# Kernel optimization log

Hardware: AMD Instinct MI355X
Metric: run time of the kernel (lower is better)

Reference implementation:

```python
import jax, jax.numpy as jnp
import numpy as np

D_MODEL = 256
N_LEVELS = 4
N_HEADS = 8
N_POINTS = 4
D_HEAD = D_MODEL // N_HEADS  # 32
BATCH = 8
SHAPES = np.array([[64, 64], [32, 32], [16, 16], [8, 8]], dtype=np.int32)
LEN_IN = int((SHAPES[:, 0] * SHAPES[:, 1]).sum())  # 5440
LEN_Q = LEN_IN
STARTS = np.concatenate([[0], np.cumsum(SHAPES[:, 0] * SHAPES[:, 1])[:-1]]).astype(np.int32)


def _offset_bias():
    # faithful _reset_parameters grid init for sampling_offsets bias
    thetas = np.arange(N_HEADS, dtype=np.float64) * (2.0 * np.pi / N_HEADS)
    grid = np.stack([np.cos(thetas), np.sin(thetas)], -1)
    grid = grid / np.abs(grid).max(-1, keepdims=True)
    grid = np.tile(grid[:, None, None, :], (1, N_LEVELS, N_POINTS, 1))
    grid = grid * (np.arange(N_POINTS) + 1)[None, None, :, None]
    return jnp.asarray(grid.reshape(-1), dtype=jnp.float32)


def setup_inputs() -> dict:
    key = jax.random.key(0)
    ks = jax.random.split(key, 8)
    s = 1.0 / np.sqrt(D_MODEL)
    return {
        "query": jax.random.normal(ks[0], (BATCH, LEN_Q, D_MODEL), jnp.float32),
        "reference_points": jax.random.uniform(ks[1], (BATCH, LEN_Q, N_LEVELS, 2), jnp.float32),
        "input_flatten": jax.random.normal(ks[2], (BATCH, LEN_IN, D_MODEL), jnp.float32),
        "input_spatial_shapes": jnp.asarray(SHAPES),
        "input_level_start_index": jnp.asarray(STARTS),
        "W_val": jax.random.normal(ks[3], (D_MODEL, D_MODEL), jnp.float32) * s,
        "b_val": jnp.zeros((D_MODEL,), jnp.float32),
        "W_off": jax.random.normal(ks[4], (D_MODEL, N_HEADS * N_LEVELS * N_POINTS * 2), jnp.float32) * 0.01,
        "b_off": _offset_bias(),
        "W_attn": jax.random.normal(ks[5], (D_MODEL, N_HEADS * N_LEVELS * N_POINTS), jnp.float32) * s,
        "b_attn": jnp.zeros((N_HEADS * N_LEVELS * N_POINTS,), jnp.float32),
        "W_out": jax.random.normal(ks[6], (D_MODEL, D_MODEL), jnp.float32) * s,
        "b_out": jnp.zeros((D_MODEL,), jnp.float32),
    }


def _ms_deform_attn_core(value, shapes_np, starts_np, sampling_locations, attention_weights):
    # value: (N, Lin, Hn, d); sampling_locations: (N, Lq, Hn, L, P, 2) in [0,1]
    # attention_weights: (N, Lq, Hn, L, P)
    n, lq = sampling_locations.shape[:2]
    value_t = jnp.transpose(value, (0, 2, 1, 3))  # (N, Hn, Lin, d)
    out = jnp.zeros((n, N_HEADS, lq, value.shape[-1]), value.dtype)
    for lvl in range(N_LEVELS):
        H, W = int(shapes_np[lvl, 0]), int(shapes_np[lvl, 1])
        st = int(starts_np[lvl])
        v = value_t[:, :, st:st + H * W]  # (N, Hn, H*W, d)
        loc = jnp.transpose(sampling_locations[:, :, :, lvl], (0, 2, 1, 3, 4))  # (N, Hn, Lq, P, 2)
        x = loc[..., 0] * W - 0.5
        y = loc[..., 1] * H - 0.5
        x0 = jnp.floor(x).astype(jnp.int32)
        y0 = jnp.floor(y).astype(jnp.int32)
        lx = x - x0
        ly = y - y0
        x1, y1 = x0 + 1, y0 + 1

        def gather(yc, xc):
            valid = (yc >= 0) & (yc < H) & (xc >= 0) & (xc < W)
            idx = jnp.clip(yc, 0, H - 1) * W + jnp.clip(xc, 0, W - 1)
            idx = idx.reshape(n, N_HEADS, -1)  # (N, Hn, Lq*P)
            g = jnp.take_along_axis(v, idx[..., None], axis=2)  # (N, Hn, Lq*P, d)
            return g * valid.reshape(n, N_HEADS, -1, 1)

        w00 = ((1 - lx) * (1 - ly)).reshape(n, N_HEADS, -1, 1)
        w01 = (lx * (1 - ly)).reshape(n, N_HEADS, -1, 1)
        w10 = ((1 - lx) * ly).reshape(n, N_HEADS, -1, 1)
        w11 = (lx * ly).reshape(n, N_HEADS, -1, 1)
        samp = (gather(y0, x0) * w00 + gather(y0, x1) * w01 +
                gather(y1, x0) * w10 + gather(y1, x1) * w11)
        samp = samp.reshape(n, N_HEADS, lq, N_POINTS, -1)
        aw = jnp.transpose(attention_weights[:, :, :, lvl], (0, 2, 1, 3))  # (N, Hn, Lq, P)
        out = out + (samp * aw[..., None]).sum(axis=3)
    return jnp.transpose(out, (0, 2, 1, 3)).reshape(n, lq, -1)


def reference(query, reference_points, input_flatten, input_spatial_shapes,
              input_level_start_index, W_val, b_val, W_off, b_off,
              W_attn, b_attn, W_out, b_out):
    shapes_np = np.asarray(input_spatial_shapes)
    starts_np = np.asarray(input_level_start_index)
    n, lq, _ = query.shape
    lin = input_flatten.shape[1]

    value = (input_flatten @ W_val + b_val).reshape(n, lin, N_HEADS, D_HEAD)
    off = (query @ W_off + b_off).reshape(n, lq, N_HEADS, N_LEVELS, N_POINTS, 2)
    attn = jax.nn.softmax((query @ W_attn + b_attn).reshape(n, lq, N_HEADS, N_LEVELS * N_POINTS), axis=-1)
    attn = attn.reshape(n, lq, N_HEADS, N_LEVELS, N_POINTS)

    # normalizer: (L, 2) as [W, H]
    normalizer = jnp.stack([input_spatial_shapes[:, 1], input_spatial_shapes[:, 0]], -1).astype(query.dtype)
    loc = reference_points[:, :, None, :, None, :] + off / normalizer[None, None, None, :, None, :]

    out = _ms_deform_attn_core(value, shapes_np, starts_np, loc, attn)
    return out @ W_out + b_out
```

## Files before the change

### kernel.cpp

```cpp
#include <hip/hip_runtime.h>

typedef unsigned short ushort;
typedef unsigned int uint;
typedef __bf16 bf16x8 __attribute__((ext_vector_type(8)));
typedef float floatx4 __attribute__((ext_vector_type(4)));
typedef ushort ushort8 __attribute__((ext_vector_type(8)));

constexpr int LQ = 5440;
constexpr int ROWS = 43520;

__device__ __forceinline__ ushort f2b(float f) {
  union { float f; uint i; } v; v.f = f;
  uint r = v.i + 0x7FFFu + ((v.i >> 16) & 1u);
  return (ushort)(r >> 16);
}
__device__ __forceinline__ float blo(uint u) {
  union { uint i; float f; } v; v.i = u << 16; return v.f;
}
__device__ __forceinline__ float bhi(uint u) {
  union { uint i; float f; } v; v.i = u & 0xFFFF0000u; return v.f;
}

__global__ __launch_bounds__(256) void wcast_kernel(
    const float* __restrict__ Wv, const float* __restrict__ Wo,
    const float* __restrict__ Wa, const float* __restrict__ Wu,
    ushort* __restrict__ Wt) {
  int k = threadIdx.x;
  int n = blockIdx.x;
  int m = blockIdx.y;
  const float* src = (m == 0) ? Wv : (m == 1) ? Wo : (m == 2) ? Wa : Wu;
  int N = (m == 2) ? 128 : 256;
  if (n >= N) return;
  size_t off = (size_t)m * 65536 - ((m == 3) ? 32768 : 0);
  Wt[off + (size_t)n * 256 + k] = f2b(src[(size_t)k * N + n]);
}

template<bool F2B>
__device__ __forceinline__ void mfma_tile128(
    const void* __restrict__ Av, const ushort* __restrict__ Bt,
    int row_base, int n0, ushort* At, ushort* Bs, floatx4 (&acc)[4][4]) {
  const int t = threadIdx.x;
  const int lane = t & 63, wv = t >> 6;
  const int quad = lane >> 4, l15 = lane & 15;
  const int mt0 = (wv >> 1) * 4, nt0 = (wv & 1) * 4;
#pragma unroll
  for (int i = 0; i < 4; ++i)
#pragma unroll
    for (int j = 0; j < 4; ++j) acc[i][j] = floatx4{0.f, 0.f, 0.f, 0.f};

  for (int k0 = 0; k0 < 256; k0 += 32) {
#pragma unroll
    for (int i = 0; i < 2; ++i) {
      int item = t + 256 * i;
      int r = item >> 2, q = item & 3;
      int slot = ((r >> 4) * 64 + q * 16 + (r & 15)) * 8;
      if (F2B) {
        const float* ap = (const float*)Av + (size_t)(row_base + r) * 256 + k0 + q * 8;
        float4 a0 = *(const float4*)ap, a1 = *(const float4*)(ap + 4);
        ushort8 u;
        u[0] = f2b(a0.x); u[1] = f2b(a0.y); u[2] = f2b(a0.z); u[3] = f2b(a0.w);
        u[4] = f2b(a1.x); u[5] = f2b(a1.y); u[6] = f2b(a1.z); u[7] = f2b(a1.w);
        *(ushort8*)&At[slot] = u;
      } else {
        const ushort* ap = (const ushort*)Av + (size_t)(row_base + r) * 256 + k0 + q * 8;
        *(ushort8*)&At[slot] = *(const ushort8*)ap;
      }
    }
#pragma unroll
    for (int i = 0; i < 2; ++i) {
      int item = t + 256 * i;
      int nr = item >> 2, q = item & 3;
      int slot = ((nr >> 4) * 64 + q * 16 + (nr & 15)) * 8;
      *(ushort8*)&Bs[slot] = *(const ushort8*)(Bt + (size_t)(n0 + nr) * 256 + k0 + q * 8);
    }
    __syncthreads();
    bf16x8 af[4], bfv[4];
#pragma unroll
    for (int ti = 0; ti < 4; ++ti)
      af[ti] = *(const bf16x8*)&At[((mt0 + ti) * 64 + lane) * 8];
#pragma unroll
    for (int tj = 0; tj < 4; ++tj)
      bfv[tj] = *(const bf16x8*)&Bs[((nt0 + tj) * 64 + lane) * 8];
#pragma unroll
    for (int ti = 0; ti < 4; ++ti)
#pragma unroll
      for (int tj = 0; tj < 4; ++tj)
        acc[ti][tj] = __builtin_amdgcn_mfma_f32_16x16x32_bf16(af[ti], bfv[tj], acc[ti][tj], 0, 0, 0);
    __syncthreads();
  }
}

__global__ __launch_bounds__(256) void gemm_val_kernel(
    const float* __restrict__ X, const ushort* __restrict__ WtV,
    const float* __restrict__ bval, ushort* __restrict__ value16) {
  __shared__ ushort At[8192];
  __shared__ ushort Bs[8192];
  floatx4 acc[4][4];
  int row_base = blockIdx.x * 128, n0 = blockIdx.y * 128;
  mfma_tile128<true>(X, WtV, row_base, n0, At, Bs, acc);
  const int t = threadIdx.x, lane = t & 63, wv = t >> 6;
  const int quad = lane >> 4, l15 = lane & 15;
  const int mt0 = (wv >> 1) * 4, nt0 = (wv & 1) * 4;
#pragma unroll
  for (int tj = 0; tj < 4; ++tj) {
    int gcol = n0 + (nt0 + tj) * 16 + l15;
    float b = bval[gcol];
#pragma unroll
    for (int ti = 0; ti < 4; ++ti)
#pragma unroll
      for (int reg = 0; reg < 4; ++reg) {
        int grow = row_base + (mt0 + ti) * 16 + quad * 4 + reg;
        value16[(size_t)grow * 256 + gcol] = f2b(acc[ti][tj][reg] + b);
      }
  }
}

__global__ __launch_bounds__(256) void gemm_oa_kernel(
    const float* __restrict__ Q, const ushort* __restrict__ WtOA,
    const float* __restrict__ boff, const float* __restrict__ battn,
    const float* __restrict__ refp, uint4* __restrict__ tblq) {
  __shared__ ushort At[2048];
  __shared__ ushort Bs[12288];
  const int t = threadIdx.x;
  const int lane = t & 63, wv = t >> 6;
  const int quad = lane >> 4, l15 = lane & 15;
  int row_base = blockIdx.x * 64;
  floatx4 accO[4][4];
  floatx4 accA[2][4];
#pragma unroll
  for (int p = 0; p < 4; ++p)
#pragma unroll
    for (int ti = 0; ti < 4; ++ti) accO[p][ti] = floatx4{0.f, 0.f, 0.f, 0.f};
#pragma unroll
  for (int q = 0; q < 2; ++q)
#pragma unroll
    for (int ti = 0; ti < 4; ++ti) accA[q][ti] = floatx4{0.f, 0.f, 0.f, 0.f};

  for (int k0 = 0; k0 < 256; k0 += 32) {
    {
      int r = t >> 2, q = t & 3;
      const float* ap = Q + (size_t)(row_base + r) * 256 + k0 + q * 8;
      float4 a0 = *(const float4*)ap, a1 = *(const float4*)(ap + 4);
      ushort8 u;
      u[0] = f2b(a0.x); u[1] = f2b(a0.y); u[2] = f2b(a0.z); u[3] = f2b(a0.w);
      u[4] = f2b(a1.x); u[5] = f2b(a1.y); u[6] = f2b(a1.z); u[7] = f2b(a1.w);
      *(ushort8*)&At[((r >> 4) * 64 + q * 16 + (r & 15)) * 8] = u;
    }
#pragma unroll
    for (int i = 0; i < 6; ++i) {
      int item = t + 256 * i;
      int nr = item >> 2, q = item & 3;
      *(ushort8*)&Bs[((nr >> 4) * 64 + q * 16 + (nr & 15)) * 8] =
          *(const ushort8*)(WtOA + (size_t)nr * 256 + k0 + q * 8);
    }
    __syncthreads();
    bf16x8 af[4];
#pragma unroll
    for (int ti = 0; ti < 4; ++ti)
      af[ti] = *(const bf16x8*)&At[(ti * 64 + lane) * 8];
#pragma unroll
    for (int p = 0; p < 4; ++p) {
      bf16x8 bf = *(const bf16x8*)&Bs[(((4 * wv + p)) * 64 + lane) * 8];
#pragma unroll
      for (int ti = 0; ti < 4; ++ti)
        accO[p][ti] = __builtin_amdgcn_mfma_f32_16x16x32_bf16(af[ti], bf, accO[p][ti], 0, 0, 0);
    }
#pragma unroll
    for (int q = 0; q < 2; ++q) {
      bf16x8 bf = *(const bf16x8*)&Bs[((16 + 2 * wv + q) * 64 + lane) * 8];
#pragma unroll
      for (int ti = 0; ti < 4; ++ti)
        accA[q][ti] = __builtin_amdgcn_mfma_f32_16x16x32_bf16(af[ti], bf, accA[q][ti], 0, 0, 0);
    }
    __syncthreads();
  }

  float boO[4], boA[2];
#pragma unroll
  for (int p = 0; p < 4; ++p) boO[p] = boff[(4 * wv + p) * 16 + l15];
#pragma unroll
  for (int q = 0; q < 2; ++q) boA[q] = battn[(2 * wv + q) * 16 + l15];
  const int lp = l15, l = lp >> 2;
  const int wd = 64 >> l;
  const int st = (l == 0) ? 0 : (l == 1) ? 4096 : (l == 2) ? 5120 : 5376;
  const float lw = (float)wd;
  const int src = (quad << 4) | (2 * (lp & 7));

#pragma unroll
  for (int ti = 0; ti < 4; ++ti)
#pragma unroll
    for (int reg = 0; reg < 4; ++reg) {
      int grow = row_base + ti * 16 + quad * 4 + reg;
      float rx = refp[(size_t)grow * 8 + l * 2];
      float ry = refp[(size_t)grow * 8 + l * 2 + 1];
#pragma unroll
      for (int hh = 0; hh < 2; ++hh) {
        int h = 2 * wv + hh;
        float xa = accA[hh][ti][reg] + boA[hh];
        float m = xa;
        m = fmaxf(m, __shfl_xor(m, 1, 64));
        m = fmaxf(m, __shfl_xor(m, 2, 64));
        m = fmaxf(m, __shfl_xor(m, 4, 64));
        m = fmaxf(m, __shfl_xor(m, 8, 64));
        float e = __expf(xa - m);
        float ssum = e;
        ssum += __shfl_xor(ssum, 1, 64);
        ssum += __shfl_xor(ssum, 2, 64);
        ssum += __shfl_xor(ssum, 4, 64);
        ssum += __shfl_xor(ssum, 8, 64);
        float aw = e / ssum;
        float v0 = accO[2 * hh][ti][reg] + boO[2 * hh];
        float v1 = accO[2 * hh + 1][ti][reg] + boO[2 * hh + 1];
        float x_lo = __shfl(v0, src, 64),     x_hi = __shfl(v1, src, 64);
        float y_lo = __shfl(v0, src | 1, 64), y_hi = __shfl(v1, src | 1, 64);
        float xo = (lp < 8) ? x_lo : x_hi;
        float yo = (lp < 8) ? y_lo : y_hi;
        float X = rx * lw + xo - 0.5f;
        float Y = ry * lw + yo - 0.5f;
        float fx = floorf(X), fy = floorf(Y);
        float lx = X - fx, ly = Y - fy;
        int x0 = (int)fx, y0 = (int)fy, x1 = x0 + 1, y1 = y0 + 1;
        int cx0 = min(max(x0, 0), wd - 1), cx1 = min(max(x1, 0), wd - 1);
        int cy0 = min(max(y0, 0), wd - 1), cy1 = min(max(y1, 0), wd - 1);
        float vx0 = (x0 >= 0 && x0 < wd) ? 1.f : 0.f;
        float vx1 = (x1 >= 0 && x1 < wd) ? 1.f : 0.f;
        float vy0 = (y0 >= 0 && y0 < wd) ? 1.f : 0.f;
        float vy1 = (y1 >= 0 && y1 < wd) ? 1.f : 0.f;
        float g00 = (1.f - lx) * (1.f - ly) * vx0 * vy0 * aw;
        float g01 = lx * (1.f - ly) * vx1 * vy0 * aw;
        float g10 = (1.f - lx) * ly * vx0 * vy1 * aw;
        float g11 = lx * ly * vx1 * vy1 * aw;
        uint i00 = st + cy0 * wd + cx0, i01 = st + cy0 * wd + cx1;
        uint i10 = st + cy1 * wd + cx0, i11 = st + cy1 * wd + cx1;
        uint4 ov;
        ov.x = i00 | (i01 << 16);
        ov.y = i10 | (i11 << 16);
        ov.z = (uint)f2b(g00) | ((uint)f2b(g01) << 16);
        ov.w = (uint)f2b(g10) | ((uint)f2b(g11) << 16);
        tblq[((size_t)grow * 8 + h) * 16 + lp] = ov;
      }
    }
}

__global__ __launch_bounds__(512) void core_kernel(
    const ushort* __restrict__ value16, const uint4* __restrict__ tblq,
    uint* __restrict__ coreo32) {
  const int bx = blockIdx.x;
  const int b = bx & 7;
  const int brow = b * LQ + (bx >> 3);
  const int t = threadIdx.x;
  const int h = t >> 6, lane = t & 63;
  const int s = lane >> 3, g = lane & 7;
  const size_t sbase = ((size_t)brow * 8 + h) * 16;
  uint4 sl0 = tblq[sbase + s];
  uint4 sl1 = tblq[sbase + s + 8];
  const uint2* vb = (const uint2*)value16 + (size_t)b * (LQ * 64) + h * 8 + g;
  float a0 = 0.f, a1 = 0.f, a2 = 0.f, a3 = 0.f;
#pragma unroll
  for (int lpi = 0; lpi < 2; ++lpi) {
    uint4 sl = lpi ? sl1 : sl0;
    uint2 v00 = vb[(size_t)(sl.x & 0xFFFFu) * 64];
    uint2 v01 = vb[(size_t)(sl.x >> 16) * 64];
    uint2 v10 = vb[(size_t)(sl.y & 0xFFFFu) * 64];
    uint2 v11 = vb[(size_t)(sl.y >> 16) * 64];
    float w00 = blo(sl.z), w01 = bhi(sl.z), w10 = blo(sl.w), w11 = bhi(sl.w);
    a0 = fmaf(w00, blo(v00.x), a0); a1 = fmaf(w00, bhi(v00.x), a1);
    a2 = fmaf(w00, blo(v00.y), a2); a3 = fmaf(w00, bhi(v00.y), a3);
    a0 = fmaf(w01, blo(v01.x), a0); a1 = fmaf(w01, bhi(v01.x), a1);
    a2 = fmaf(w01, blo(v01.y), a2); a3 = fmaf(w01, bhi(v01.y), a3);
    a0 = fmaf(w10, blo(v10.x), a0); a1 = fmaf(w10, bhi(v10.x), a1);
    a2 = fmaf(w10, blo(v10.y), a2); a3 = fmaf(w10, bhi(v10.y), a3);
    a0 = fmaf(w11, blo(v11.x), a0); a1 = fmaf(w11, bhi(v11.x), a1);
    a2 = fmaf(w11, blo(v11.y), a2); a3 = fmaf(w11, bhi(v11.y), a3);
  }
#pragma unroll
  for (int m = 8; m <= 32; m <<= 1) {
    a0 += __shfl_xor(a0, m, 64);
    a1 += __shfl_xor(a1, m, 64);
    a2 += __shfl_xor(a2, m, 64);
    a3 += __shfl_xor(a3, m, 64);
  }
  if (s == 0) {
    uint2 o;
    o.x = (uint)f2b(a0) | ((uint)f2b(a1) << 16);
    o.y = (uint)f2b(a2) | ((uint)f2b(a3) << 16);
    *(uint2*)(coreo32 + (size_t)brow * 128 + h * 16 + g * 2) = o;
  }
}

__global__ __launch_bounds__(256) void gemm_out_kernel(
    const ushort* __restrict__ C, const ushort* __restrict__ WtU,
    const float* __restrict__ bout, float* __restrict__ out) {
  __shared__ ushort At[8192];
  __shared__ ushort Bs[8192];
  floatx4 acc[4][4];
  int row_base = blockIdx.x * 128, n0 = blockIdx.y * 128;
  mfma_tile128<false>(C, WtU, row_base, n0, At, Bs, acc);
  const int t = threadIdx.x, lane = t & 63, wv = t >> 6;
  const int quad = lane >> 4, l15 = lane & 15;
  const int mt0 = (wv >> 1) * 4, nt0 = (wv & 1) * 4;
#pragma unroll
  for (int tj = 0; tj < 4; ++tj) {
    int gcol = n0 + (nt0 + tj) * 16 + l15;
    float b = bout[gcol];
#pragma unroll
    for (int ti = 0; ti < 4; ++ti)
#pragma unroll
      for (int reg = 0; reg < 4; ++reg) {
        int grow = row_base + (mt0 + ti) * 16 + quad * 4 + reg;
        out[(size_t)grow * 256 + gcol] = acc[ti][tj][reg] + b;
      }
  }
}

extern "C" void kernel_launch(void* const* d_in, const int* in_sizes, int n_in,
                              void* d_out, int out_size, void* d_ws, size_t ws_size,
                              hipStream_t stream) {
  const float* query  = (const float*)d_in[0];
  const float* refp   = (const float*)d_in[1];
  const float* inpf   = (const float*)d_in[2];
  const float* W_val  = (const float*)d_in[5];
  const float* b_val  = (const float*)d_in[6];
  const float* W_off  = (const float*)d_in[7];
  const float* b_off  = (const float*)d_in[8];
  const float* W_attn = (const float*)d_in[9];
  const float* b_attn = (const float*)d_in[10];
  const float* W_out  = (const float*)d_in[11];
  const float* b_out  = (const float*)d_in[12];

  char* ws = (char*)d_ws;
  ushort* Wt    = (ushort*)ws;
  ushort* value = (ushort*)(ws + 1048576);
  uint4*  tbl   = (uint4*)(ws + 23330816);
  ushort* coreo = (ushort*)(ws + 112459776);

  dim3 blk(256);
  wcast_kernel   <<<dim3(256, 4), blk, 0, stream>>>(W_val, W_off, W_attn, W_out, Wt);
  gemm_val_kernel<<<dim3(340, 2), blk, 0, stream>>>(inpf, Wt, b_val, value);
  gemm_oa_kernel <<<dim3(680), blk, 0, stream>>>(query, Wt + 65536, b_off, b_attn, refp, tbl);
  core_kernel    <<<dim3(ROWS), dim3(512), 0, stream>>>(value, tbl, (uint*)coreo);
  gemm_out_kernel<<<dim3(340, 2), blk, 0, stream>>>(coreo, Wt + 163840, b_out, (float*)d_out);
}
```

Measured before the change: 340.2 us.

## Shrink GEMM tiles, split offset/attention GEMM by head pair, two rows per core block

The value and output projections move from 128x128 to 64x128 tiles, which doubles the block count. The offset/attention GEMM is split across four head-pair blocks per 64-row tile, which cuts its shared memory and accumulator registers. The sampling kernel now handles two query rows per block, halving the block count and amortising launch overhead across more loads in flight. The aim is better occupancy and GPU fill, at the cost of more redundant A-tile loads and query bf16 conversion in the split GEMMs.

New measurement: 334.7 us. No clear change (-1.6%).

```diff
diff --git a/kernel.cpp b/kernel.cpp
--- a/kernel.cpp
+++ b/kernel.cpp
@@ -36,23 +36,19 @@
 }
 
 template<bool F2B>
-__device__ __forceinline__ void mfma_tile128(
+__device__ __forceinline__ void tile64_mainloop(
     const void* __restrict__ Av, const ushort* __restrict__ Bt,
-    int row_base, int n0, ushort* At, ushort* Bs, floatx4 (&acc)[4][4]) {
+    int row_base, int n0, ushort* At, ushort* Bs, floatx4 (&acc)[4][2]) {
   const int t = threadIdx.x;
   const int lane = t & 63, wv = t >> 6;
-  const int quad = lane >> 4, l15 = lane & 15;
-  const int mt0 = (wv >> 1) * 4, nt0 = (wv & 1) * 4;
 #pragma unroll
   for (int i = 0; i < 4; ++i)
 #pragma unroll
-    for (int j = 0; j < 4; ++j) acc[i][j] = floatx4{0.f, 0.f, 0.f, 0.f};
+    for (int j = 0; j < 2; ++j) acc[i][j] = floatx4{0.f, 0.f, 0.f, 0.f};
 
   for (int k0 = 0; k0 < 256; k0 += 32) {
-#pragma unroll
-    for (int i = 0; i < 2; ++i) {
-      int item = t + 256 * i;
-      int r = item >> 2, q = item & 3;
+    {
+      int r = t >> 2, q = t & 3;
       int slot = ((r >> 4) * 64 + q * 16 + (r & 15)) * 8;
       if (F2B) {
         const float* ap = (const float*)Av + (size_t)(row_base + r) * 256 + k0 + q * 8;
@@ -74,43 +70,42 @@
       *(ushort8*)&Bs[slot] = *(const ushort8*)(Bt + (size_t)(n0 + nr) * 256 + k0 + q * 8);
     }
     __syncthreads();
-    bf16x8 af[4], bfv[4];
+    bf16x8 af[4], bf[2];
 #pragma unroll
     for (int ti = 0; ti < 4; ++ti)
-      af[ti] = *(const bf16x8*)&At[((mt0 + ti) * 64 + lane) * 8];
-#pragma unroll
-    for (int tj = 0; tj < 4; ++tj)
-      bfv[tj] = *(const bf16x8*)&Bs[((nt0 + tj) * 64 + lane) * 8];
+      af[ti] = *(const bf16x8*)&At[(ti * 64 + lane) * 8];
+#pragma unroll
+    for (int tjj = 0; tjj < 2; ++tjj)
+      bf[tjj] = *(const bf16x8*)&Bs[((2 * wv + tjj) * 64 + lane) * 8];
 #pragma unroll
     for (int ti = 0; ti < 4; ++ti)
 #pragma unroll
-      for (int tj = 0; tj < 4; ++tj)
-        acc[ti][tj] = __builtin_amdgcn_mfma_f32_16x16x32_bf16(af[ti], bfv[tj], acc[ti][tj], 0, 0, 0);
+      for (int tjj = 0; tjj < 2; ++tjj)
+        acc[ti][tjj] = __builtin_amdgcn_mfma_f32_16x16x32_bf16(af[ti], bf[tjj], acc[ti][tjj], 0, 0, 0);
     __syncthreads();
   }
 }
 
-__global__ __launch_bounds__(256) void gemm_val_kernel(
+__global__ __launch_bounds__(256) void gemm_val64(
     const float* __restrict__ X, const ushort* __restrict__ WtV,
     const float* __restrict__ bval, ushort* __restrict__ value16) {
-  __shared__ ushort At[8192];
-  __shared__ ushort Bs[8192];
-  floatx4 acc[4][4];
-  int row_base = blockIdx.x * 128, n0 = blockIdx.y * 128;
-  mfma_tile128<true>(X, WtV, row_base, n0, At, Bs, acc);
+  __shared__ ushort At[2048];
+  __shared__ ushort Bs[4096];
+  floatx4 acc[4][2];
+  int row_base = blockIdx.x * 64, n0 = blockIdx.y * 128;
+  tile64_mainloop<true>(X, WtV, row_base, n0, At, Bs, acc);
   const int t = threadIdx.x, lane = t & 63, wv = t >> 6;
   const int quad = lane >> 4, l15 = lane & 15;
-  const int mt0 = (wv >> 1) * 4, nt0 = (wv & 1) * 4;
-#pragma unroll
-  for (int tj = 0; tj < 4; ++tj) {
-    int gcol = n0 + (nt0 + tj) * 16 + l15;
+#pragma unroll
+  for (int tjj = 0; tjj < 2; ++tjj) {
+    int gcol = n0 + (2 * wv + tjj) * 16 + l15;
     float b = bval[gcol];
 #pragma unroll
     for (int ti = 0; ti < 4; ++ti)
 #pragma unroll
       for (int reg = 0; reg < 4; ++reg) {
-        int grow = row_base + (mt0 + ti) * 16 + quad * 4 + reg;
-        value16[(size_t)grow * 256 + gcol] = f2b(acc[ti][tj][reg] + b);
+        int grow = row_base + ti * 16 + quad * 4 + reg;
+        value16[(size_t)grow * 256 + gcol] = f2b(acc[ti][tjj][reg] + b);
       }
   }
 }
@@ -120,21 +115,18 @@
     const float* __restrict__ boff, const float* __restrict__ battn,
     const float* __restrict__ refp, uint4* __restrict__ tblq) {
   __shared__ ushort At[2048];
-  __shared__ ushort Bs[12288];
+  __shared__ ushort Bs[3072];
   const int t = threadIdx.x;
   const int lane = t & 63, wv = t >> 6;
   const int quad = lane >> 4, l15 = lane & 15;
-  int row_base = blockIdx.x * 64;
-  floatx4 accO[4][4];
-  floatx4 accA[2][4];
-#pragma unroll
-  for (int p = 0; p < 4; ++p)
-#pragma unroll
-    for (int ti = 0; ti < 4; ++ti) accO[p][ti] = floatx4{0.f, 0.f, 0.f, 0.f};
-#pragma unroll
-  for (int q = 0; q < 2; ++q)
-#pragma unroll
-    for (int ti = 0; ti < 4; ++ti) accA[q][ti] = floatx4{0.f, 0.f, 0.f, 0.f};
+  const int bx = blockIdx.x;
+  const int row_base = (bx % 680) * 64;
+  const int hp = bx / 680;
+  floatx4 accO[4], accA[2];
+#pragma unroll
+  for (int p = 0; p < 4; ++p) accO[p] = floatx4{0.f, 0.f, 0.f, 0.f};
+#pragma unroll
+  for (int q = 0; q < 2; ++q) accA[q] = floatx4{0.f, 0.f, 0.f, 0.f};
 
   for (int k0 = 0; k0 < 256; k0 += 32) {
     {
@@ -147,99 +139,93 @@
       *(ushort8*)&At[((r >> 4) * 64 + q * 16 + (r & 15)) * 8] = u;
     }
 #pragma unroll
-    for (int i = 0; i < 6; ++i) {
+    for (int i = 0; i < 2; ++i) {
       int item = t + 256 * i;
-      int nr = item >> 2, q = item & 3;
-      *(ushort8*)&Bs[((nr >> 4) * 64 + q * 16 + (nr & 15)) * 8] =
-          *(const ushort8*)(WtOA + (size_t)nr * 256 + k0 + q * 8);
+      if (item < 384) {
+        int nrl = item >> 2, q = item & 3;
+        int grow_ = (nrl < 64) ? (hp * 64 + nrl) : (256 + hp * 32 + (nrl - 64));
+        *(ushort8*)&Bs[((nrl >> 4) * 64 + q * 16 + (nrl & 15)) * 8] =
+            *(const ushort8*)(WtOA + (size_t)grow_ * 256 + k0 + q * 8);
+      }
     }
     __syncthreads();
-    bf16x8 af[4];
-#pragma unroll
-    for (int ti = 0; ti < 4; ++ti)
-      af[ti] = *(const bf16x8*)&At[(ti * 64 + lane) * 8];
+    bf16x8 af = *(const bf16x8*)&At[(wv * 64 + lane) * 8];
 #pragma unroll
     for (int p = 0; p < 4; ++p) {
-      bf16x8 bf = *(const bf16x8*)&Bs[(((4 * wv + p)) * 64 + lane) * 8];
-#pragma unroll
-      for (int ti = 0; ti < 4; ++ti)
-        accO[p][ti] = __builtin_amdgcn_mfma_f32_16x16x32_bf16(af[ti], bf, accO[p][ti], 0, 0, 0);
+      bf16x8 bf = *(const bf16x8*)&Bs[(p * 64 + lane) * 8];
+      accO[p] = __builtin_amdgcn_mfma_f32_16x16x32_bf16(af, bf, accO[p], 0, 0, 0);
     }
 #pragma unroll
     for (int q = 0; q < 2; ++q) {
-      bf16x8 bf = *(const bf16x8*)&Bs[((16 + 2 * wv + q) * 64 + lane) * 8];
-#pragma unroll
-      for (int ti = 0; ti < 4; ++ti)
-        accA[q][ti] = __builtin_amdgcn_mfma_f32_16x16x32_bf16(af[ti], bf, accA[q][ti], 0, 0, 0);
+      bf16x8 bf = *(const bf16x8*)&Bs[((4 + q) * 64 + lane) * 8];
+      accA[q] = __builtin_amdgcn_mfma_f32_16x16x32_bf16(af, bf, accA[q], 0, 0, 0);
     }
     __syncthreads();
   }
 
-  float boO[4], boA[2];
-#pragma unroll
-  for (int p = 0; p < 4; ++p) boO[p] = boff[(4 * wv + p) * 16 + l15];
-#pragma unroll
-  for (int q = 0; q < 2; ++q) boA[q] = battn[(2 * wv + q) * 16 + l15];
   const int lp = l15, l = lp >> 2;
   const int wd = 64 >> l;
   const int st = (l == 0) ? 0 : (l == 1) ? 4096 : (l == 2) ? 5120 : 5376;
   const float lw = (float)wd;
   const int src = (quad << 4) | (2 * (lp & 7));
-
-#pragma unroll
-  for (int ti = 0; ti < 4; ++ti)
-#pragma unroll
-    for (int reg = 0; reg < 4; ++reg) {
-      int grow = row_base + ti * 16 + quad * 4 + reg;
-      float rx = refp[(size_t)grow * 8 + l * 2];
-      float ry = refp[(size_t)grow * 8 + l * 2 + 1];
-#pragma unroll
-      for (int hh = 0; hh < 2; ++hh) {
-        int h = 2 * wv + hh;
-        float xa = accA[hh][ti][reg] + boA[hh];
-        float m = xa;
-        m = fmaxf(m, __shfl_xor(m, 1, 64));
-        m = fmaxf(m, __shfl_xor(m, 2, 64));
-        m = fmaxf(m, __shfl_xor(m, 4, 64));
-        m = fmaxf(m, __shfl_xor(m, 8, 64));
-        float e = __expf(xa - m);
-        float ssum = e;
-        ssum += __shfl_xor(ssum, 1, 64);
-        ssum += __shfl_xor(ssum, 2, 64);
-        ssum += __shfl_xor(ssum, 4, 64);
-        ssum += __shfl_xor(ssum, 8, 64);
-        float aw = e / ssum;
-        float v0 = accO[2 * hh][ti][reg] + boO[2 * hh];
-        float v1 = accO[2 * hh + 1][ti][reg] + boO[2 * hh + 1];
-        float x_lo = __shfl(v0, src, 64),     x_hi = __shfl(v1, src, 64);
-        float y_lo = __shfl(v0, src | 1, 64), y_hi = __shfl(v1, src | 1, 64);
-        float xo = (lp < 8) ? x_lo : x_hi;
-        float yo = (lp < 8) ? y_lo : y_hi;
-        float X = rx * lw + xo - 0.5f;
-        float Y = ry * lw + yo - 0.5f;
-        float fx = floorf(X), fy = floorf(Y);
-        float lx = X - fx, ly = Y - fy;
-        int x0 = (int)fx, y0 = (int)fy, x1 = x0 + 1, y1 = y0 + 1;
-        int cx0 = min(max(x0, 0), wd - 1), cx1 = min(max(x1, 0), wd - 1);
-        int cy0 = min(max(y0, 0), wd - 1), cy1 = min(max(y1, 0), wd - 1);
-        float vx0 = (x0 >= 0 && x0 < wd) ? 1.f : 0.f;
-        float vx1 = (x1 >= 0 && x1 < wd) ? 1.f : 0.f;
-        float vy0 = (y0 >= 0 && y0 < wd) ? 1.f : 0.f;
-        float vy1 = (y1 >= 0 && y1 < wd) ? 1.f : 0.f;
-        float g00 = (1.f - lx) * (1.f - ly) * vx0 * vy0 * aw;
-        float g01 = lx * (1.f - ly) * vx1 * vy0 * aw;
-        float g10 = (1.f - lx) * ly * vx0 * vy1 * aw;
-        float g11 = lx * ly * vx1 * vy1 * aw;
-        uint i00 = st + cy0 * wd + cx0, i01 = st + cy0 * wd + cx1;
-        uint i10 = st + cy1 * wd + cx0, i11 = st + cy1 * wd + cx1;
-        uint4 ov;
-        ov.x = i00 | (i01 << 16);
-        ov.y = i10 | (i11 << 16);
-        ov.z = (uint)f2b(g00) | ((uint)f2b(g01) << 16);
-        ov.w = (uint)f2b(g10) | ((uint)f2b(g11) << 16);
-        tblq[((size_t)grow * 8 + h) * 16 + lp] = ov;
-      }
-    }
+  float boO[4], boA[2];
+#pragma unroll
+  for (int p = 0; p < 4; ++p) boO[p] = boff[(4 * hp + p) * 16 + l15];
+#pragma unroll
+  for (int q = 0; q < 2; ++q) boA[q] = battn[(2 * hp + q) * 16 + l15];
+
+#pragma unroll
+  for (int reg = 0; reg < 4; ++reg) {
+    int grow = row_base + wv * 16 + quad * 4 + reg;
+    float rx = refp[(size_t)grow * 8 + l * 2];
+    float ry = refp[(size_t)grow * 8 + l * 2 + 1];
+#pragma unroll
+    for (int hh = 0; hh < 2; ++hh) {
+      int h = 2 * hp + hh;
+      float xa = accA[hh][reg] + boA[hh];
+      float m = xa;
+      m = fmaxf(m, __shfl_xor(m, 1, 64));
+      m = fmaxf(m, __shfl_xor(m, 2, 64));
+      m = fmaxf(m, __shfl_xor(m, 4, 64));
+      m = fmaxf(m, __shfl_xor(m, 8, 64));
+      float e = __expf(xa - m);
+      float ssum = e;
+      ssum += __shfl_xor(ssum, 1, 64);
+      ssum += __shfl_xor(ssum, 2, 64);
+      ssum += __shfl_xor(ssum, 4, 64);
+      ssum += __shfl_xor(ssum, 8, 64);
+      float aw = e / ssum;
+      float v0 = accO[2 * hh][reg] + boO[2 * hh];
+      float v1 = accO[2 * hh + 1][reg] + boO[2 * hh + 1];
+      float x_lo = __shfl(v0, src, 64),     x_hi = __shfl(v1, src, 64);
+      float y_lo = __shfl(v0, src | 1, 64), y_hi = __shfl(v1, src | 1, 64);
+      float xo = (lp < 8) ? x_lo : x_hi;
+      float yo = (lp < 8) ? y_lo : y_hi;
+      float X = rx * lw + xo - 0.5f;
+      float Y = ry * lw + yo - 0.5f;
+      float fx = floorf(X), fy = floorf(Y);
+      float lx = X - fx, ly = Y - fy;
+      int x0 = (int)fx, y0 = (int)fy, x1 = x0 + 1, y1 = y0 + 1;
+      int cx0 = min(max(x0, 0), wd - 1), cx1 = min(max(x1, 0), wd - 1);
+      int cy0 = min(max(y0, 0), wd - 1), cy1 = min(max(y1, 0), wd - 1);
+      float vx0 = (x0 >= 0 && x0 < wd) ? 1.f : 0.f;
+      float vx1 = (x1 >= 0 && x1 < wd) ? 1.f : 0.f;
+      float vy0 = (y0 >= 0 && y0 < wd) ? 1.f : 0.f;
+      float vy1 = (y1 >= 0 && y1 < wd) ? 1.f : 0.f;
+      float g00 = (1.f - lx) * (1.f - ly) * vx0 * vy0 * aw;
+      float g01 = lx * (1.f - ly) * vx1 * vy0 * aw;
+      float g10 = (1.f - lx) * ly * vx0 * vy1 * aw;
+      float g11 = lx * ly * vx1 * vy1 * aw;
+      uint i00 = st + cy0 * wd + cx0, i01 = st + cy0 * wd + cx1;
+      uint i10 = st + cy1 * wd + cx0, i11 = st + cy1 * wd + cx1;
+      uint4 ov;
+      ov.x = i00 | (i01 << 16);
+      ov.y = i10 | (i11 << 16);
+      ov.z = (uint)f2b(g00) | ((uint)f2b(g01) << 16);
+      ov.w = (uint)f2b(g10) | ((uint)f2b(g11) << 16);
+      tblq[((size_t)grow * 8 + h) * 16 + lp] = ov;
+    }
+  }
 }
 
 __global__ __launch_bounds__(512) void core_kernel(
@@ -247,68 +233,77 @@
     uint* __restrict__ coreo32) {
   const int bx = blockIdx.x;
   const int b = bx & 7;
-  const int brow = b * LQ + (bx >> 3);
+  const int pr = bx >> 3;
+  const int brow0 = b * LQ + pr * 2;
   const int t = threadIdx.x;
   const int h = t >> 6, lane = t & 63;
   const int s = lane >> 3, g = lane & 7;
-  const size_t sbase = ((size_t)brow * 8 + h) * 16;
-  uint4 sl0 = tblq[sbase + s];
-  uint4 sl1 = tblq[sbase + s + 8];
+  const size_t sb = ((size_t)brow0 * 8 + h) * 16;
+  uint4 sA0 = tblq[sb + s];
+  uint4 sA1 = tblq[sb + 8 + s];
+  uint4 sB0 = tblq[sb + 128 + s];
+  uint4 sB1 = tblq[sb + 136 + s];
   const uint2* vb = (const uint2*)value16 + (size_t)b * (LQ * 64) + h * 8 + g;
-  float a0 = 0.f, a1 = 0.f, a2 = 0.f, a3 = 0.f;
-#pragma unroll
-  for (int lpi = 0; lpi < 2; ++lpi) {
-    uint4 sl = lpi ? sl1 : sl0;
+  float a[4] = {0.f, 0.f, 0.f, 0.f};
+  float c[4] = {0.f, 0.f, 0.f, 0.f};
+
+  auto proc = [&](const uint4& sl, float* ac) {
     uint2 v00 = vb[(size_t)(sl.x & 0xFFFFu) * 64];
     uint2 v01 = vb[(size_t)(sl.x >> 16) * 64];
     uint2 v10 = vb[(size_t)(sl.y & 0xFFFFu) * 64];
     uint2 v11 = vb[(size_t)(sl.y >> 16) * 64];
     float w00 = blo(sl.z), w01 = bhi(sl.z), w10 = blo(sl.w), w11 = bhi(sl.w);
-    a0 = fmaf(w00, blo(v00.x), a0); a1 = fmaf(w00, bhi(v00.x), a1);
-    a2 = fmaf(w00, blo(v00.y), a2); a3 = fmaf(w00, bhi(v00.y), a3);
-    a0 = fmaf(w01, blo(v01.x), a0); a1 = fmaf(w01, bhi(v01.x), a1);
-    a2 = fmaf(w01, blo(v01.y), a2); a3 = fmaf(w01, bhi(v01.y), a3);
-    a0 = fmaf(w10, blo(v10.x), a0); a1 = fmaf(w10, bhi(v10.x), a1);
-    a2 = fmaf(w10, blo(v10.y), a2); a3 = fmaf(w10, bhi(v10.y), a3);
-    a0 = fmaf(w11, blo(v11.x), a0); a1 = fmaf(w11, bhi(v11.x), a1);
-    a2 = fmaf(w11, blo(v11.y), a2); a3 = fmaf(w11, bhi(v11.y), a3);
-  }
+    ac[0] = fmaf(w00, blo(v00.x), ac[0]); ac[1] = fmaf(w00, bhi(v00.x), ac[1]);
+    ac[2] = fmaf(w00, blo(v00.y), ac[2]); ac[3] = fmaf(w00, bhi(v00.y), ac[3]);
+    ac[0] = fmaf(w01, blo(v01.x), ac[0]); ac[1] = fmaf(w01, bhi(v01.x), ac[1]);
+    ac[2] = fmaf(w01, blo(v01.y), ac[2]); ac[3] = fmaf(w01, bhi(v01.y), ac[3]);
+    ac[0] = fmaf(w10, blo(v10.x), ac[0]); ac[1] = fmaf(w10, bhi(v10.x), ac[1]);
+    ac[2] = fmaf(w10, blo(v10.y), ac[2]); ac[3] = fmaf(w10, bhi(v10.y), ac[3]);
+    ac[0] = fmaf(w11, blo(v11.x), ac[0]); ac[1] = fmaf(w11, bhi(v11.x), ac[1]);
+    ac[2] = fmaf(w11, blo(v11.y), ac[2]); ac[3] = fmaf(w11, bhi(v11.y), ac[3]);
+  };
+  proc(sA0, a); proc(sA1, a);
+  proc(sB0, c); proc(sB1, c);
+
 #pragma unroll
   for (int m = 8; m <= 32; m <<= 1) {
-    a0 += __shfl_xor(a0, m, 64);
-    a1 += __shfl_xor(a1, m, 64);
-    a2 += __shfl_xor(a2, m, 64);
-    a3 += __shfl_xor(a3, m, 64);
+#pragma unroll
+    for (int i = 0; i < 4; ++i) {
+      a[i] += __shfl_xor(a[i], m, 64);
+      c[i] += __shfl_xor(c[i], m, 64);
+    }
   }
   if (s == 0) {
-    uint2 o;
-    o.x = (uint)f2b(a0) | ((uint)f2b(a1) << 16);
-    o.y = (uint)f2b(a2) | ((uint)f2b(a3) << 16);
-    *(uint2*)(coreo32 + (size_t)brow * 128 + h * 16 + g * 2) = o;
-  }
-}
-
-__global__ __launch_bounds__(256) void gemm_out_kernel(
+    uint2 o0, o1;
+    o0.x = (uint)f2b(a[0]) | ((uint)f2b(a[1]) << 16);
+    o0.y = (uint)f2b(a[2]) | ((uint)f2b(a[3]) << 16);
+    o1.x = (uint)f2b(c[0]) | ((uint)f2b(c[1]) << 16);
+    o1.y = (uint)f2b(c[2]) | ((uint)f2b(c[3]) << 16);
+    *(uint2*)(coreo32 + (size_t)brow0 * 128 + h * 16 + g * 2) = o0;
+    *(uint2*)(coreo32 + (size_t)(brow0 + 1) * 128 + h * 16 + g * 2) = o1;
+  }
+}
+
+__global__ __launch_bounds__(256) void gemm_out64(
     const ushort* __restrict__ C, const ushort* __restrict__ WtU,
     const float* __restrict__ bout, float* __restrict__ out) {
-  __shared__ ushort At[8192];
-  __shared__ ushort Bs[8192];
-  floatx4 acc[4][4];
-  int row_base = blockIdx.x * 128, n0 = blockIdx.y * 128;
-  mfma_tile128<false>(C, WtU, row_base, n0, At, Bs, acc);
+  __shared__ ushort At[2048];
+  __shared__ ushort Bs[4096];
+  floatx4 acc[4][2];
+  int row_base = blockIdx.x * 64, n0 = blockIdx.y * 128;
+  tile64_mainloop<false>(C, WtU, row_base, n0, At, Bs, acc);
   const int t = threadIdx.x, lane = t & 63, wv = t >> 6;
   const int quad = lane >> 4, l15 = lane & 15;
-  const int mt0 = (wv >> 1) * 4, nt0 = (wv & 1) * 4;
-#pragma unroll
-  for (int tj = 0; tj < 4; ++tj) {
-    int gcol = n0 + (nt0 + tj) * 16 + l15;
+#pragma unroll
+  for (int tjj = 0; tjj < 2; ++tjj) {
+    int gcol = n0 + (2 * wv + tjj) * 16 + l15;
     float b = bout[gcol];
 #pragma unroll
     for (int ti = 0; ti < 4; ++ti)
 #pragma unroll
       for (int reg = 0; reg < 4; ++reg) {
-        int grow = row_base + (mt0 + ti) * 16 + quad * 4 + reg;
-        out[(size_t)grow * 256 + gcol] = acc[ti][tj][reg] + b;
+        int grow = row_base + ti * 16 + quad * 4 + reg;
+        out[(size_t)grow * 256 + gcol] = acc[ti][tjj][reg] + b;
       }
   }
 }
@@ -335,9 +330,9 @@
   ushort* coreo = (ushort*)(ws + 112459776);
 
   dim3 blk(256);
-  wcast_kernel   <<<dim3(256, 4), blk, 0, stream>>>(W_val, W_off, W_attn, W_out, Wt);
-  gemm_val_kernel<<<dim3(340, 2), blk, 0, stream>>>(inpf, Wt, b_val, value);
-  gemm_oa_kernel <<<dim3(680), blk, 0, stream>>>(query, Wt + 65536, b_off, b_attn, refp, tbl);
-  core_kernel    <<<dim3(ROWS), dim3(512), 0, stream>>>(value, tbl, (uint*)coreo);
-  gemm_out_kernel<<<dim3(340, 2), blk, 0, stream>>>(coreo, Wt + 163840, b_out, (float*)d_out);
-}
+  wcast_kernel<<<dim3(256, 4), blk, 0, stream>>>(W_val, W_off, W_attn, W_out, Wt);
+  gemm_val64  <<<dim3(680, 2), blk, 0, stream>>>(inpf, Wt, b_val, value);
+  gemm_oa_kernel<<<dim3(2720), blk, 0, stream>>>(query, Wt + 65536, b_off, b_attn, refp, tbl);
+  core_kernel <<<dim3(21760), dim3(512), 0, stream>>>(value, tbl, (uint*)coreo);
+  gemm_out64  <<<dim3(680, 2), blk, 0, stream>>>(coreo, Wt + 163840, b_out, (float*)d_out);
+}
```
